# Kernel optimization log

Measured on AMD Instinct MI355X. Metric: run time of the kernel, lower is better.

The kernel has to match this reference:

```python
import jax, jax.numpy as jnp
import numpy as np

B, S, D, H, F = 2, 2048, 1024, 16, 4096
DH = D // H


def setup_inputs() -> dict:
    key = jax.random.key(0)
    ks = jax.random.split(key, 8)
    scale = 0.02
    def nrm(k, shape):
        return jax.random.normal(k, shape, jnp.float32) * scale
    return {
        "x": jax.random.normal(ks[0], (B, S, D), jnp.float32),
        "ln1_g": jnp.ones((D,), jnp.float32),
        "ln1_b": jnp.zeros((D,), jnp.float32),
        "wq": nrm(ks[1], (D, D)), "bq": jnp.zeros((D,), jnp.float32),
        "wk": nrm(ks[2], (D, D)), "bk": jnp.zeros((D,), jnp.float32),
        "wv": nrm(ks[3], (D, D)), "bv": jnp.zeros((D,), jnp.float32),
        "wo": nrm(ks[4], (D, D)), "bo": jnp.zeros((D,), jnp.float32),
        "ln2_g": jnp.ones((D,), jnp.float32),
        "ln2_b": jnp.zeros((D,), jnp.float32),
        "w1": nrm(ks[5], (D, F)), "b1": jnp.zeros((F,), jnp.float32),
        "w2": nrm(ks[6], (F, D)), "b2": jnp.zeros((D,), jnp.float32),
    }


def _layernorm(x, g, b, eps=1e-5):
    m = jnp.mean(x, axis=-1, keepdims=True)
    v = jnp.var(x, axis=-1, keepdims=True)
    return (x - m) / jnp.sqrt(v + eps) * g + b


def reference(x, ln1_g, ln1_b, wq, bq, wk, bk, wv, bv, wo, bo,
              ln2_g, ln2_b, w1, b1, w2, b2):
    # GPT2Block forward, prefill path (state=None): K/V = ln_1(x), causal mask.
    Bx, Sx, Dx = x.shape
    h = _layernorm(x, ln1_g, ln1_b)

    def heads(t):  # [B,S,D] -> [B,H,S,DH]
        return t.reshape(Bx, Sx, H, DH).transpose(0, 2, 1, 3)

    q = heads(h @ wq + bq)
    k = heads(h @ wk + bk)
    v = heads(h @ wv + bv)

    scores = jnp.einsum('bhqd,bhkd->bhqk', q, k) / jnp.sqrt(jnp.float32(DH))
    # masked_softmax: key position < valid_len (= query_pos+1) kept; else -1e6
    causal = jnp.arange(Sx)[None, :] <= jnp.arange(Sx)[:, None]  # [S,S]
    scores = jnp.where(causal, scores, jnp.float32(-1e6))
    attn_w = jax.nn.softmax(scores, axis=-1)

    o = jnp.einsum('bhqk,bhkd->bhqd', attn_w, v)
    o = o.transpose(0, 2, 1, 3).reshape(Bx, Sx, Dx)
    attn_out = o @ wo + bo

    add1 = x + attn_out  # dropout inactive (eval)
    h2 = _layernorm(add1, ln2_g, ln2_b)
    mlp = jax.nn.gelu(h2 @ w1 + b1, approximate=False) @ w2 + b2
    return add1 + mlp
```

## Files before the change

### kernel.cpp

```cpp
#include <hip/hip_runtime.h>
#include <hip/hip_bf16.h>


#define BDIM 1024
#define SEQ 2048
#define NH 16
#define DHEAD 64
#define FDIM 4096
#define QKVD 3072

typedef __attribute__((ext_vector_type(8))) short short8v;
typedef __attribute__((ext_vector_type(4))) float floatx4;

__device__ __forceinline__ unsigned short f2bf(float f) {
    unsigned int u = __float_as_uint(f);
    unsigned int r = u + 0x7FFFu + ((u >> 16) & 1u);
    return (unsigned short)(r >> 16);
}
__device__ __forceinline__ unsigned int pack2bf(float a, float b) {
    return (unsigned int)f2bf(a) | ((unsigned int)f2bf(b) << 16);
}

__device__ __forceinline__ void load16_lds(const unsigned short* g, short* l) {
    __builtin_amdgcn_global_load_lds((const __attribute__((address_space(1))) void*)g,
                                     (__attribute__((address_space(3))) void*)l, 16, 0, 0);
}

__global__ __launch_bounds__(256) void transpose_all(const float* __restrict__ wq,
                                                     const float* __restrict__ wk,
                                                     const float* __restrict__ wv,
                                                     const float* __restrict__ wo,
                                                     const float* __restrict__ w1,
                                                     const float* __restrict__ w2,
                                                     unsigned short* __restrict__ qkvT,
                                                     unsigned short* __restrict__ woT,
                                                     unsigned short* __restrict__ w1T,
                                                     unsigned short* __restrict__ w2T) {
    const int g = blockIdx.x;
    const float* W;
    unsigned short* Wt;
    int K, N, tx, ty;
    if (g < 4096) {
        const int w = g >> 10, tile = g & 1023;
        tx = tile & 31; ty = tile >> 5; K = 1024; N = 1024;
        W = (w == 0) ? wq : (w == 1) ? wk : (w == 2) ? wv : wo;
        Wt = (w == 3) ? woT : qkvT + (size_t)w * 1024 * 1024;
    } else if (g < 8192) {
        const int tile = g - 4096;
        tx = tile & 127; ty = tile >> 7; K = 1024; N = 4096;
        W = w1; Wt = w1T;
    } else {
        const int tile = g - 8192;
        tx = tile & 31; ty = tile >> 5; K = 4096; N = 1024;
        W = w2; Wt = w2T;
    }
    __shared__ float tile[32][33];
    const int t = threadIdx.x;
    const int r = t >> 3, c4 = (t & 7) * 4;
    const int n0 = tx * 32, k0 = ty * 32;
    float4 p = *(const float4*)(W + (size_t)(k0 + r) * N + n0 + c4);
    tile[r][c4 + 0] = p.x;
    tile[r][c4 + 1] = p.y;
    tile[r][c4 + 2] = p.z;
    tile[r][c4 + 3] = p.w;
    __syncthreads();
    ushort4 ou;
    ou.x = f2bf(tile[c4 + 0][r]);
    ou.y = f2bf(tile[c4 + 1][r]);
    ou.z = f2bf(tile[c4 + 2][r]);
    ou.w = f2bf(tile[c4 + 3][r]);
    *(ushort4*)(Wt + (size_t)(n0 + r) * K + k0 + c4) = ou;
}

__global__ void concat_bias(const float* __restrict__ a, const float* __restrict__ b,
                            const float* __restrict__ c, float* __restrict__ out) {
    int i = blockIdx.x * 256 + threadIdx.x;
    out[i] = (i < 1024) ? a[i] : (i < 2048 ? b[i - 1024] : c[i - 2048]);
}

__global__ __launch_bounds__(256) void ln_kernel(const float* __restrict__ x,
                                                 const float* __restrict__ g,
                                                 const float* __restrict__ bb,
                                                 unsigned short* __restrict__ out) {
    const int row = blockIdx.x;
    const int t = threadIdx.x;
    const int c = t * 4;
    float4 p = *(const float4*)(x + (size_t)row * BDIM + c);
    float s = p.x + p.y + p.z + p.w;
    float sq = p.x * p.x + p.y * p.y + p.z * p.z + p.w * p.w;
    for (int off = 1; off < 64; off <<= 1) {
        s += __shfl_xor(s, off);
        sq += __shfl_xor(sq, off);
    }
    __shared__ float ssum[4], ssq[4];
    const int wave = t >> 6, lane = t & 63;
    if (lane == 0) { ssum[wave] = s; ssq[wave] = sq; }
    __syncthreads();
    s = ssum[0] + ssum[1] + ssum[2] + ssum[3];
    sq = ssq[0] + ssq[1] + ssq[2] + ssq[3];
    const float mean = s * (1.0f / BDIM);
    const float var = sq * (1.0f / BDIM) - mean * mean;
    const float rstd = rsqrtf(var + 1e-5f);
    float4 gg = *(const float4*)(g + c);
    float4 bv = *(const float4*)(bb + c);
    ushort4 o;
    o.x = f2bf((p.x - mean) * rstd * gg.x + bv.x);
    o.y = f2bf((p.y - mean) * rstd * gg.y + bv.y);
    o.z = f2bf((p.z - mean) * rstd * gg.z + bv.z);
    o.w = f2bf((p.w - mean) * rstd * gg.w + bv.w);
    *(ushort4*)(out + (size_t)row * BDIM + c) = o;
}

template <int BN, int RES, int GELU, int OBF16, int QSCALE = 0, int VOUT = 0>
__global__ __launch_bounds__(256, 3) void mfma_gemm(const unsigned short* __restrict__ A,
                                                    const unsigned short* __restrict__ Bt,
                                                    const float* __restrict__ bias,
                                                    const float* __restrict__ res,
                                                    void* __restrict__ Cv,
                                                    unsigned short* __restrict__ vtout,
                                                    int M, int N, int K) {
    constexpr int MI = (BN == 128) ? 4 : 2;
    constexpr int CHB = BN * 4;
    __shared__ short As[2][128 * 32];
    __shared__ short Bs[2][BN * 32];
    const int t = threadIdx.x;
    const int wave = t >> 6, lane = t & 63;
    const int m0 = blockIdx.y * 128, n0 = blockIdx.x * BN;
    const int wmrow = (BN == 128) ? (wave & 1) * 64 : wave * 32;
    const int wnrow = (BN == 128) ? (wave >> 1) * 64 : 0;
    const int mlane = lane & 15, quad = lane >> 4;

    floatx4 acc[MI][4];
#pragma unroll
    for (int mi = 0; mi < MI; ++mi)
#pragma unroll
        for (int ni = 0; ni < 4; ++ni) {
            floatx4 z = {0.0f, 0.0f, 0.0f, 0.0f};
            acc[mi][ni] = z;
        }

    for (int k0 = 0; k0 < K; k0 += 64) {
        __syncthreads();
#pragma unroll
        for (int j = 0; j < 4; ++j) {
            const int c = j * 256 + t;
            const int hh = c >> 9, cc = c & 511;
            load16_lds(A + (size_t)(m0 + (cc >> 2)) * K + k0 + hh * 32 + (cc & 3) * 8,
                       &As[hh][cc * 8]);
        }
#pragma unroll
        for (int j = 0; j < CHB / 128; ++j) {
            const int c = j * 256 + t;
            const int hh = c / CHB, cc = c % CHB;
            load16_lds(Bt + (size_t)(n0 + (cc >> 2)) * K + k0 + hh * 32 + (cc & 3) * 8,
                       &Bs[hh][cc * 8]);
        }
        __syncthreads();
#pragma unroll
        for (int hh = 0; hh < 2; ++hh) {
            short8v a[MI], b[4];
#pragma unroll
            for (int mi = 0; mi < MI; ++mi)
                a[mi] = *(const short8v*)&As[hh][(wmrow + mi * 16 + mlane) * 32 + quad * 8];
#pragma unroll
            for (int ni = 0; ni < 4; ++ni)
                b[ni] = *(const short8v*)&Bs[hh][(wnrow + ni * 16 + mlane) * 32 + quad * 8];
#pragma unroll
            for (int mi = 0; mi < MI; ++mi)
#pragma unroll
                for (int ni = 0; ni < 4; ++ni)
                    acc[mi][ni] = __builtin_amdgcn_mfma_f32_16x16x32_bf16(a[mi], b[ni], acc[mi][ni], 0, 0, 0);
        }
    }
#pragma unroll
    for (int mi = 0; mi < MI; ++mi) {
#pragma unroll
        for (int ni = 0; ni < 4; ++ni) {
            const int col = n0 + wnrow + ni * 16 + mlane;
            const float bv = bias[col];
            const int row0 = m0 + wmrow + mi * 16 + quad * 4;
            if (VOUT && col >= 2048) {
                const int vd = col - 2048;
                const int bb = row0 >> 11, ss = row0 & 2047;
                uint2 pk;
                pk.x = pack2bf(acc[mi][ni][0] + bv, acc[mi][ni][1] + bv);
                pk.y = pack2bf(acc[mi][ni][2] + bv, acc[mi][ni][3] + bv);
                *(uint2*)(vtout + ((size_t)(bb * NH + (vd >> 6)) * DHEAD + (vd & 63)) * SEQ + ss) = pk;
            } else {
#pragma unroll
                for (int rg = 0; rg < 4; ++rg) {
                    const int row = row0 + rg;
                    float v = acc[mi][ni][rg] + bv;
                    if (RES) v += res[(size_t)row * N + col];
                    if (GELU) v = 0.5f * v * (1.0f + erff(v * 0.70710678118654752f));
                    if (QSCALE && col < 1024) v *= 0.125f;
                    if (OBF16)
                        ((unsigned short*)Cv)[(size_t)row * N + col] = f2bf(v);
                    else
                        ((float*)Cv)[(size_t)row * N + col] = v;
                }
            }
        }
    }
}

__global__ __launch_bounds__(256) void attn_kernel(const unsigned short* __restrict__ qkv,
                                                   const unsigned short* __restrict__ vt,
                                                   unsigned short* __restrict__ o) {
    const int g = blockIdx.x;
    const int qt = (g < 256) ? (15 - (g >> 5)) : ((g - 256) >> 5);
    const int hb = g & 31;
    const int h = hb & 15, b = hb >> 4;
    const int t = threadIdx.x;
    const int wave = t >> 6, lane = t & 63;
    const int mlane = lane & 15, quad = lane >> 4;
    const int wq0 = qt * 128 + wave * 32;
    const size_t bS = (size_t)b * SEQ;

    __shared__ unsigned short Ks[64][72];
    __shared__ unsigned short Vs[64][72];
    __shared__ __align__(16) unsigned short plds[4][2][16][72];

    short8v qf[2][2];
#pragma unroll
    for (int ng = 0; ng < 2; ++ng) {
        const unsigned short* qrow = qkv + (bS + wq0 + ng * 16 + mlane) * QKVD + h * DHEAD;
        qf[ng][0] = *(const short8v*)(qrow + quad * 8);
        qf[ng][1] = *(const short8v*)(qrow + 32 + quad * 8);
    }

    const unsigned short* kbase = qkv + bS * QKVD + 1024 + h * DHEAD;
    const unsigned short* vbase = vt + ((size_t)(b * NH + h)) * DHEAD * SEQ;

    const int sr = t >> 3, so = (t & 7) * 8;
    const unsigned short* kg0 = kbase + (size_t)sr * QKVD + so;
    const unsigned short* kg1 = kbase + (size_t)(32 + sr) * QKVD + so;
    const unsigned short* vg0 = vbase + (size_t)sr * SEQ + so;
    const unsigned short* vg1 = vbase + (size_t)(32 + sr) * SEQ + so;

    floatx4 ot[2][4];
#pragma unroll
    for (int ng = 0; ng < 2; ++ng)
#pragma unroll
        for (int mt = 0; mt < 4; ++mt) { floatx4 z = {0, 0, 0, 0}; ot[ng][mt] = z; }
    float m_r[2] = {-INFINITY, -INFINITY}, l_r[2] = {0.0f, 0.0f};

    const int kend = wq0 + 32;
    const int kmax = qt * 128 + 128;

    uint4 kr0 = *(const uint4*)kg0;
    uint4 kr1 = *(const uint4*)kg1;
    uint4 vr0 = *(const uint4*)vg0;
    uint4 vr1 = *(const uint4*)vg1;

    for (int k0 = 0; k0 < kmax; k0 += 64) {
        *(uint4*)&Ks[sr][so] = kr0;
        *(uint4*)&Ks[32 + sr][so] = kr1;
        *(uint4*)&Vs[sr][so] = vr0;
        *(uint4*)&Vs[32 + sr][so] = vr1;
        __syncthreads();
        if (k0 + 64 < kmax) {
            kr0 = *(const uint4*)(kg0 + (size_t)(k0 + 64) * QKVD);
            kr1 = *(const uint4*)(kg1 + (size_t)(k0 + 64) * QKVD);
            vr0 = *(const uint4*)(vg0 + (k0 + 64));
            vr1 = *(const uint4*)(vg1 + (k0 + 64));
        }
        if (k0 < kend) {
            floatx4 st[2][4];
#pragma unroll
            for (int ng = 0; ng < 2; ++ng)
#pragma unroll
                for (int kt = 0; kt < 4; ++kt) {
                    floatx4 mz = {-1e30f, -1e30f, -1e30f, -1e30f};
                    st[ng][kt] = mz;
                }
#pragma unroll
            for (int kt = 0; kt < 4; ++kt) {
                if (k0 + kt * 16 < kend) {
                    short8v kfa = *(const short8v*)&Ks[kt * 16 + mlane][quad * 8];
                    short8v kfb = *(const short8v*)&Ks[kt * 16 + mlane][32 + quad * 8];
#pragma unroll
                    for (int ng = 0; ng < 2; ++ng) {
                        floatx4 z = {0, 0, 0, 0};
                        st[ng][kt] = __builtin_amdgcn_mfma_f32_16x16x32_bf16(kfa, qf[ng][0], z, 0, 0, 0);
                        st[ng][kt] = __builtin_amdgcn_mfma_f32_16x16x32_bf16(kfb, qf[ng][1], st[ng][kt], 0, 0, 0);
                    }
                }
            }
            if (k0 + 64 >= kend) {
#pragma unroll
                for (int ng = 0; ng < 2; ++ng)
#pragma unroll
                    for (int kt = 0; kt < 4; ++kt)
#pragma unroll
                        for (int rg = 0; rg < 4; ++rg)
                            if (k0 + kt * 16 + quad * 4 + rg > wq0 + ng * 16 + mlane)
                                st[ng][kt][rg] = -1e30f;
            }
#pragma unroll
            for (int ng = 0; ng < 2; ++ng) {
                float tm = st[ng][0][0];
#pragma unroll
                for (int kt = 0; kt < 4; ++kt)
#pragma unroll
                    for (int rg = 0; rg < 4; ++rg) tm = fmaxf(tm, st[ng][kt][rg]);
                tm = fmaxf(tm, __shfl_xor(tm, 16));
                tm = fmaxf(tm, __shfl_xor(tm, 32));
                const float newm = fmaxf(m_r[ng], tm);
                const float alpha = __expf(m_r[ng] - newm);
                m_r[ng] = newm;
                float p[4][4], psum = 0.0f;
#pragma unroll
                for (int kt = 0; kt < 4; ++kt)
#pragma unroll
                    for (int rg = 0; rg < 4; ++rg) {
                        p[kt][rg] = __expf(st[ng][kt][rg] - newm);
                        psum += p[kt][rg];
                    }
                psum += __shfl_xor(psum, 16);
                psum += __shfl_xor(psum, 32);
                l_r[ng] = l_r[ng] * alpha + psum;
#pragma unroll
                for (int mt = 0; mt < 4; ++mt)
#pragma unroll
                    for (int rg = 0; rg < 4; ++rg) ot[ng][mt][rg] *= alpha;
#pragma unroll
                for (int kt = 0; kt < 4; ++kt) {
                    uint2 pk;
                    pk.x = pack2bf(p[kt][0], p[kt][1]);
                    pk.y = pack2bf(p[kt][2], p[kt][3]);
                    *(uint2*)&plds[wave][ng][mlane][kt * 16 + quad * 4] = pk;
                }
            }
#pragma unroll
            for (int kh = 0; kh < 2; ++kh) {
                if (k0 + kh * 32 < kend) {
                    short8v vf[4];
#pragma unroll
                    for (int mt = 0; mt < 4; ++mt)
                        vf[mt] = *(const short8v*)&Vs[mt * 16 + mlane][kh * 32 + quad * 8];
#pragma unroll
                    for (int ng = 0; ng < 2; ++ng) {
                        short8v pf = *(const short8v*)&plds[wave][ng][mlane][kh * 32 + quad * 8];
#pragma unroll
                        for (int mt = 0; mt < 4; ++mt)
                            ot[ng][mt] = __builtin_amdgcn_mfma_f32_16x16x32_bf16(vf[mt], pf, ot[ng][mt], 0, 0, 0);
                    }
                }
            }
        }
        __syncthreads();
    }

#pragma unroll
    for (int ng = 0; ng < 2; ++ng) {
        const float inv = 1.0f / l_r[ng];
        unsigned short* orow = o + (bS + wq0 + ng * 16 + mlane) * BDIM + h * DHEAD;
#pragma unroll
        for (int mt = 0; mt < 4; ++mt) {
            uint2 pk;
            pk.x = pack2bf(ot[ng][mt][0] * inv, ot[ng][mt][1] * inv);
            pk.y = pack2bf(ot[ng][mt][2] * inv, ot[ng][mt][3] * inv);
            *(uint2*)(orow + mt * 16 + quad * 4) = pk;
        }
    }
}

extern "C" void kernel_launch(void* const* d_in, const int* in_sizes, int n_in,
                              void* d_out, int out_size, void* d_ws, size_t ws_size,
                              hipStream_t stream) {
    const int M = 2 * SEQ;

    const float* x = (const float*)d_in[0];
    const float* ln1_g = (const float*)d_in[1];
    const float* ln1_b = (const float*)d_in[2];
    const float* wq = (const float*)d_in[3];
    const float* bq = (const float*)d_in[4];
    const float* wk = (const float*)d_in[5];
    const float* bk = (const float*)d_in[6];
    const float* wv = (const float*)d_in[7];
    const float* bv = (const float*)d_in[8];
    const float* wo = (const float*)d_in[9];
    const float* bo = (const float*)d_in[10];
    const float* ln2_g = (const float*)d_in[11];
    const float* ln2_b = (const float*)d_in[12];
    const float* w1 = (const float*)d_in[13];
    const float* b1 = (const float*)d_in[14];
    const float* w2 = (const float*)d_in[15];
    const float* b2 = (const float*)d_in[16];

    char* wsb = (char*)d_ws;
    unsigned short* qkv = (unsigned short*)wsb;
    unsigned short* ffn = (unsigned short*)wsb;
    unsigned short* vt = (unsigned short*)(wsb + (24u << 20));
    unsigned short* hbuf = (unsigned short*)(wsb + (32u << 20));
    float* add1 = (float*)(wsb + (40u << 20));
    unsigned short* h2 = (unsigned short*)(wsb + (56u << 20));
    unsigned short* qkvT = (unsigned short*)(wsb + (64u << 20));
    unsigned short* woT = (unsigned short*)(wsb + (70u << 20));
    unsigned short* w1T = (unsigned short*)(wsb + (72u << 20));
    unsigned short* w2T = (unsigned short*)(wsb + (80u << 20));
    float* bqkv = (float*)(wsb + (88u << 20));

    transpose_all<<<12288, 256, 0, stream>>>(wq, wk, wv, wo, w1, w2, qkvT, woT, w1T, w2T);
    concat_bias<<<12, 256, 0, stream>>>(bq, bk, bv, bqkv);

    ln_kernel<<<M, 256, 0, stream>>>(x, ln1_g, ln1_b, hbuf);

    mfma_gemm<128, 0, 0, 1, 1, 1><<<dim3(QKVD / 128, M / 128), 256, 0, stream>>>(
        hbuf, qkvT, bqkv, nullptr, qkv, vt, M, QKVD, 1024);

    attn_kernel<<<512, 256, 0, stream>>>(qkv, vt, hbuf);

    mfma_gemm<64, 1, 0, 0><<<dim3(1024 / 64, M / 128), 256, 0, stream>>>(
        hbuf, woT, bo, x, add1, nullptr, M, 1024, 1024);

    ln_kernel<<<M, 256, 0, stream>>>(add1, ln2_g, ln2_b, h2);

    mfma_gemm<128, 0, 1, 1><<<dim3(FDIM / 128, M / 128), 256, 0, stream>>>(
        h2, w1T, b1, nullptr, ffn, nullptr, M, FDIM, 1024);

    mfma_gemm<64, 1, 0, 0><<<dim3(1024 / 64, M / 128), 256, 0, stream>>>(
        ffn, w2T, b2, add1, (float*)d_out, nullptr, M, 1024, FDIM);
}
```

Baseline: 359.5 us.

## Restructure attention to 8 waves of 16 rows with swizzled LDS and lazy rescale

The attention kernel now launches 512 threads per block, so each of 8 waves owns 16 query rows instead of 32. LDS tiles drop their padding and use XOR swizzling to avoid bank conflicts. The softmax switches to exp2 with log2(e) folded into the Q scale, and skips the running-max rescale unless the max rises by more than 8. This aims to raise occupancy and latency hiding and to cut exp and rescale work, at the cost of more waves sharing each K/V tile and the extra masking and swizzle arithmetic.

```diff
diff --git a/kernel.cpp b/kernel.cpp
--- a/kernel.cpp
+++ b/kernel.cpp
@@ -193,7 +193,7 @@
                     float v = acc[mi][ni][rg] + bv;
                     if (RES) v += res[(size_t)row * N + col];
                     if (GELU) v = 0.5f * v * (1.0f + erff(v * 0.70710678118654752f));
-                    if (QSCALE && col < 1024) v *= 0.125f;
+                    if (QSCALE && col < 1024) v *= 0.18033688011112042f;
                     if (OBF16)
                         ((unsigned short*)Cv)[(size_t)row * N + col] = f2bf(v);
                     else
@@ -204,9 +204,9 @@
     }
 }
 
-__global__ __launch_bounds__(256) void attn_kernel(const unsigned short* __restrict__ qkv,
-                                                   const unsigned short* __restrict__ vt,
-                                                   unsigned short* __restrict__ o) {
+__global__ __launch_bounds__(512, 4) void attn_kernel(const unsigned short* __restrict__ qkv,
+                                                      const unsigned short* __restrict__ vt,
+                                                      unsigned short* __restrict__ o) {
     const int g = blockIdx.x;
     const int qt = (g < 256) ? (15 - (g >> 5)) : ((g - 256) >> 5);
     const int hb = g & 31;
@@ -214,123 +214,106 @@
     const int t = threadIdx.x;
     const int wave = t >> 6, lane = t & 63;
     const int mlane = lane & 15, quad = lane >> 4;
-    const int wq0 = qt * 128 + wave * 32;
+    const int msw = mlane & 7;
+    const int wq0 = qt * 128 + wave * 16;
     const size_t bS = (size_t)b * SEQ;
 
-    __shared__ unsigned short Ks[64][72];
-    __shared__ unsigned short Vs[64][72];
-    __shared__ __align__(16) unsigned short plds[4][2][16][72];
-
-    short8v qf[2][2];
-#pragma unroll
-    for (int ng = 0; ng < 2; ++ng) {
-        const unsigned short* qrow = qkv + (bS + wq0 + ng * 16 + mlane) * QKVD + h * DHEAD;
-        qf[ng][0] = *(const short8v*)(qrow + quad * 8);
-        qf[ng][1] = *(const short8v*)(qrow + 32 + quad * 8);
+    __shared__ unsigned short Ks[64][64];
+    __shared__ unsigned short Vs[64][64];
+    __shared__ __align__(16) unsigned short plds[8][16][64];
+
+    short8v qf0, qf1;
+    {
+        const unsigned short* qrow = qkv + (bS + wq0 + mlane) * QKVD + h * DHEAD;
+        qf0 = *(const short8v*)(qrow + quad * 8);
+        qf1 = *(const short8v*)(qrow + 32 + quad * 8);
     }
 
     const unsigned short* kbase = qkv + bS * QKVD + 1024 + h * DHEAD;
     const unsigned short* vbase = vt + ((size_t)(b * NH + h)) * DHEAD * SEQ;
 
-    const int sr = t >> 3, so = (t & 7) * 8;
-    const unsigned short* kg0 = kbase + (size_t)sr * QKVD + so;
-    const unsigned short* kg1 = kbase + (size_t)(32 + sr) * QKVD + so;
-    const unsigned short* vg0 = vbase + (size_t)sr * SEQ + so;
-    const unsigned short* vg1 = vbase + (size_t)(32 + sr) * SEQ + so;
-
-    floatx4 ot[2][4];
-#pragma unroll
-    for (int ng = 0; ng < 2; ++ng)
-#pragma unroll
-        for (int mt = 0; mt < 4; ++mt) { floatx4 z = {0, 0, 0, 0}; ot[ng][mt] = z; }
-    float m_r[2] = {-INFINITY, -INFINITY}, l_r[2] = {0.0f, 0.0f};
-
-    const int kend = wq0 + 32;
+    const int sr = t >> 3, sc = t & 7;
+    const int ssw = (sc ^ (sr & 7)) * 8;
+    const unsigned short* kg = kbase + (size_t)sr * QKVD + sc * 8;
+    const unsigned short* vg = vbase + (size_t)sr * SEQ + sc * 8;
+
+    floatx4 ot[4];
+#pragma unroll
+    for (int mt = 0; mt < 4; ++mt) { floatx4 z = {0, 0, 0, 0}; ot[mt] = z; }
+    float m_r = -INFINITY, l_r = 0.0f;
+
+    const int kend = wq0 + 16;
     const int kmax = qt * 128 + 128;
 
-    uint4 kr0 = *(const uint4*)kg0;
-    uint4 kr1 = *(const uint4*)kg1;
-    uint4 vr0 = *(const uint4*)vg0;
-    uint4 vr1 = *(const uint4*)vg1;
+    uint4 kr = *(const uint4*)kg;
+    uint4 vr = *(const uint4*)vg;
 
     for (int k0 = 0; k0 < kmax; k0 += 64) {
-        *(uint4*)&Ks[sr][so] = kr0;
-        *(uint4*)&Ks[32 + sr][so] = kr1;
-        *(uint4*)&Vs[sr][so] = vr0;
-        *(uint4*)&Vs[32 + sr][so] = vr1;
+        *(uint4*)&Ks[sr][ssw] = kr;
+        *(uint4*)&Vs[sr][ssw] = vr;
         __syncthreads();
         if (k0 + 64 < kmax) {
-            kr0 = *(const uint4*)(kg0 + (size_t)(k0 + 64) * QKVD);
-            kr1 = *(const uint4*)(kg1 + (size_t)(k0 + 64) * QKVD);
-            vr0 = *(const uint4*)(vg0 + (k0 + 64));
-            vr1 = *(const uint4*)(vg1 + (k0 + 64));
+            kr = *(const uint4*)(kg + (size_t)(k0 + 64) * QKVD);
+            vr = *(const uint4*)(vg + (k0 + 64));
         }
         if (k0 < kend) {
-            floatx4 st[2][4];
-#pragma unroll
-            for (int ng = 0; ng < 2; ++ng)
-#pragma unroll
-                for (int kt = 0; kt < 4; ++kt) {
-                    floatx4 mz = {-1e30f, -1e30f, -1e30f, -1e30f};
-                    st[ng][kt] = mz;
-                }
+            floatx4 st[4];
 #pragma unroll
             for (int kt = 0; kt < 4; ++kt) {
                 if (k0 + kt * 16 < kend) {
-                    short8v kfa = *(const short8v*)&Ks[kt * 16 + mlane][quad * 8];
-                    short8v kfb = *(const short8v*)&Ks[kt * 16 + mlane][32 + quad * 8];
-#pragma unroll
-                    for (int ng = 0; ng < 2; ++ng) {
-                        floatx4 z = {0, 0, 0, 0};
-                        st[ng][kt] = __builtin_amdgcn_mfma_f32_16x16x32_bf16(kfa, qf[ng][0], z, 0, 0, 0);
-                        st[ng][kt] = __builtin_amdgcn_mfma_f32_16x16x32_bf16(kfb, qf[ng][1], st[ng][kt], 0, 0, 0);
-                    }
+                    short8v kfa = *(const short8v*)&Ks[kt * 16 + mlane][(quad ^ msw) * 8];
+                    short8v kfb = *(const short8v*)&Ks[kt * 16 + mlane][((quad + 4) ^ msw) * 8];
+                    floatx4 z = {0, 0, 0, 0};
+                    st[kt] = __builtin_amdgcn_mfma_f32_16x16x32_bf16(kfa, qf0, z, 0, 0, 0);
+                    st[kt] = __builtin_amdgcn_mfma_f32_16x16x32_bf16(kfb, qf1, st[kt], 0, 0, 0);
+                } else {
+                    floatx4 mz = {-1e30f, -1e30f, -1e30f, -1e30f};
+                    st[kt] = mz;
                 }
             }
             if (k0 + 64 >= kend) {
 #pragma unroll
-                for (int ng = 0; ng < 2; ++ng)
-#pragma unroll
-                    for (int kt = 0; kt < 4; ++kt)
-#pragma unroll
-                        for (int rg = 0; rg < 4; ++rg)
-                            if (k0 + kt * 16 + quad * 4 + rg > wq0 + ng * 16 + mlane)
-                                st[ng][kt][rg] = -1e30f;
-            }
-#pragma unroll
-            for (int ng = 0; ng < 2; ++ng) {
-                float tm = st[ng][0][0];
-#pragma unroll
                 for (int kt = 0; kt < 4; ++kt)
 #pragma unroll
-                    for (int rg = 0; rg < 4; ++rg) tm = fmaxf(tm, st[ng][kt][rg]);
-                tm = fmaxf(tm, __shfl_xor(tm, 16));
-                tm = fmaxf(tm, __shfl_xor(tm, 32));
-                const float newm = fmaxf(m_r[ng], tm);
-                const float alpha = __expf(m_r[ng] - newm);
-                m_r[ng] = newm;
-                float p[4][4], psum = 0.0f;
-#pragma unroll
-                for (int kt = 0; kt < 4; ++kt)
-#pragma unroll
-                    for (int rg = 0; rg < 4; ++rg) {
-                        p[kt][rg] = __expf(st[ng][kt][rg] - newm);
-                        psum += p[kt][rg];
-                    }
-                psum += __shfl_xor(psum, 16);
-                psum += __shfl_xor(psum, 32);
-                l_r[ng] = l_r[ng] * alpha + psum;
+                    for (int rg = 0; rg < 4; ++rg)
+                        if (k0 + kt * 16 + quad * 4 + rg > wq0 + mlane)
+                            st[kt][rg] = -1e30f;
+            }
+            float tm = st[0][0];
+#pragma unroll
+            for (int kt = 0; kt < 4; ++kt)
+#pragma unroll
+                for (int rg = 0; rg < 4; ++rg) tm = fmaxf(tm, st[kt][rg]);
+            tm = fmaxf(tm, __shfl_xor(tm, 16));
+            tm = fmaxf(tm, __shfl_xor(tm, 32));
+            if (!__all(tm <= m_r + 8.0f)) {
+                const float newm = fmaxf(m_r, tm);
+                const float alpha = exp2f(m_r - newm);
+                l_r *= alpha;
 #pragma unroll
                 for (int mt = 0; mt < 4; ++mt)
 #pragma unroll
-                    for (int rg = 0; rg < 4; ++rg) ot[ng][mt][rg] *= alpha;
-#pragma unroll
-                for (int kt = 0; kt < 4; ++kt) {
-                    uint2 pk;
-                    pk.x = pack2bf(p[kt][0], p[kt][1]);
-                    pk.y = pack2bf(p[kt][2], p[kt][3]);
-                    *(uint2*)&plds[wave][ng][mlane][kt * 16 + quad * 4] = pk;
+                    for (int rg = 0; rg < 4; ++rg) ot[mt][rg] *= alpha;
+                m_r = newm;
+            }
+            float p[4][4], psum = 0.0f;
+#pragma unroll
+            for (int kt = 0; kt < 4; ++kt)
+#pragma unroll
+                for (int rg = 0; rg < 4; ++rg) {
+                    p[kt][rg] = exp2f(st[kt][rg] - m_r);
+                    psum += p[kt][rg];
                 }
+            psum += __shfl_xor(psum, 16);
+            psum += __shfl_xor(psum, 32);
+            l_r += psum;
+            char* prow = (char*)&plds[wave][mlane][0];
+#pragma unroll
+            for (int kt = 0; kt < 4; ++kt) {
+                uint2 pk;
+                pk.x = pack2bf(p[kt][0], p[kt][1]);
+                pk.y = pack2bf(p[kt][2], p[kt][3]);
+                *(uint2*)(prow + ((kt * 32 + quad * 8) ^ (msw << 4))) = pk;
             }
 #pragma unroll
             for (int kh = 0; kh < 2; ++kh) {
@@ -338,31 +321,25 @@
                     short8v vf[4];
 #pragma unroll
                     for (int mt = 0; mt < 4; ++mt)
-                        vf[mt] = *(const short8v*)&Vs[mt * 16 + mlane][kh * 32 + quad * 8];
-#pragma unroll
-                    for (int ng = 0; ng < 2; ++ng) {
-                        short8v pf = *(const short8v*)&plds[wave][ng][mlane][kh * 32 + quad * 8];
-#pragma unroll
-                        for (int mt = 0; mt < 4; ++mt)
-                            ot[ng][mt] = __builtin_amdgcn_mfma_f32_16x16x32_bf16(vf[mt], pf, ot[ng][mt], 0, 0, 0);
-                    }
+                        vf[mt] = *(const short8v*)&Vs[mt * 16 + mlane][(((kh * 4 + quad) ^ msw)) * 8];
+                    short8v pf = *(const short8v*)(prow + (((kh * 4 + quad) ^ msw) << 4));
+#pragma unroll
+                    for (int mt = 0; mt < 4; ++mt)
+                        ot[mt] = __builtin_amdgcn_mfma_f32_16x16x32_bf16(vf[mt], pf, ot[mt], 0, 0, 0);
                 }
             }
         }
         __syncthreads();
     }
 
-#pragma unroll
-    for (int ng = 0; ng < 2; ++ng) {
-        const float inv = 1.0f / l_r[ng];
-        unsigned short* orow = o + (bS + wq0 + ng * 16 + mlane) * BDIM + h * DHEAD;
-#pragma unroll
-        for (int mt = 0; mt < 4; ++mt) {
-            uint2 pk;
-            pk.x = pack2bf(ot[ng][mt][0] * inv, ot[ng][mt][1] * inv);
-            pk.y = pack2bf(ot[ng][mt][2] * inv, ot[ng][mt][3] * inv);
-            *(uint2*)(orow + mt * 16 + quad * 4) = pk;
-        }
+    const float inv = 1.0f / l_r;
+    unsigned short* orow = o + (bS + wq0 + mlane) * BDIM + h * DHEAD;
+#pragma unroll
+    for (int mt = 0; mt < 4; ++mt) {
+        uint2 pk;
+        pk.x = pack2bf(ot[mt][0] * inv, ot[mt][1] * inv);
+        pk.y = pack2bf(ot[mt][2] * inv, ot[mt][3] * inv);
+        *(uint2*)(orow + mt * 16 + quad * 4) = pk;
     }
 }
 
@@ -410,7 +387,7 @@
     mfma_gemm<128, 0, 0, 1, 1, 1><<<dim3(QKVD / 128, M / 128), 256, 0, stream>>>(
         hbuf, qkvT, bqkv, nullptr, qkv, vt, M, QKVD, 1024);
 
-    attn_kernel<<<512, 256, 0, stream>>>(qkv, vt, hbuf);
+    attn_kernel<<<512, 512, 0, stream>>>(qkv, vt, hbuf);
 
     mfma_gemm<64, 1, 0, 0><<<dim3(1024 / 64, M / 128), 256, 0, stream>>>(
         hbuf, woT, bo, x, add1, nullptr, M, 1024, 1024);
```

After: 349.2 us. 1.03x faster.
